# Kernel tuning notes

Measured on AMD Instinct MI355X. Metric: run time of the kernel, lower is better.

## Reference

```python
import jax, jax.numpy as jnp
import numpy as np

B, C, H, W = 4, 256, 56, 56
N = H * W  # 3136 tokens


def setup_inputs() -> dict:
    key = jax.random.key(0)
    ks = jax.random.split(key, 12)
    f = lambda k, s: jax.random.normal(k, s, dtype=jnp.float32)
    return {
        "feat0": f(ks[0], (B, 1, C, H, W)),
        "feat1": f(ks[1], (B, 1, C, H, W)),
        "feat2": f(ks[2], (B, 1, C, H, W)),
        "feat3": f(ks[3], (B, 1, C, H, W)),
        "hist0": jax.random.uniform(ks[4], (B, N), dtype=jnp.float32),
        "hist1": jax.random.uniform(ks[5], (B, N), dtype=jnp.float32),
        "hist2": jax.random.uniform(ks[6], (B, N), dtype=jnp.float32),
        "mask": f(ks[7], (N, N)),
        "Wv": f(ks[8], (C, C)) * 0.02,   # v_linear weight (torch layout [out,in])
        "bv": jnp.zeros((C,), jnp.float32),
        "Wl": f(ks[9], (C, 2 * C)) * 0.02,  # low_channel weight
        "bl": jnp.zeros((C,), jnp.float32),
    }


def _tokens(x5d):
    # [b,1,c,h,w] -> [b, n, c]
    b = x5d.shape[0]
    return x5d.reshape(b, C, N).transpose(0, 2, 1)


def _to5d(tok):
    # [b,n,c] -> [b,1,c,h,w]
    b = tok.shape[0]
    return tok.transpose(0, 2, 1).reshape(b, 1, C, H, W)


def reference(feat0, feat1, feat2, feat3, hist0, hist1, hist2, mask, Wv, bv, Wl, bl):
    scale = 1.0 / jnp.sqrt(jnp.float32(C))

    def stage(q_tok, feat5d):
        f = _tokens(feat5d)                                   # [b,n,c]
        corr = jnp.einsum('bnc,bmc->bnm', q_tok, f) * scale   # [b,n,n]
        p = jax.nn.softmax(corr + mask[None], axis=-1)        # masked softmax
        v = f @ Wv.T + bv                                     # v_linear
        motion = jnp.einsum('bnm,bmc->bnc', p, v)             # attention
        refined = motion + f                                  # residual
        out = jnp.concatenate([refined, f], axis=-1) @ Wl.T + bl  # low_channel
        return refined, out

    # histograms (hist0..hist2) are consumed by the original module but its
    # histogram_mask is dead code; they do not affect the math.
    q = _tokens(feat0)
    refined, out1 = stage(q, feat1)
    refined, out2 = stage(refined, feat2)
    refined, out3 = stage(refined, feat3)

    return jnp.concatenate(
        [feat0, _to5d(out1), _to5d(out2), _to5d(out3)], axis=1
    )  # [b, 4, c, h, w]
```

## Files before the change

kernel.cpp:

```cpp
#include <hip/hip_runtime.h>
#include <hip/hip_bf16.h>

#define B_   4
#define C_   256
#define N_   3136
#define QT_  196
#define NKV_ 98
#define CH_  5

typedef __attribute__((ext_vector_type(8)))  short bf16x8;
typedef __attribute__((ext_vector_type(4)))  float f32x4;
typedef __attribute__((ext_vector_type(16))) float f32x16;

#define LOG2E  1.4426950408889634f
#define SCALE2 (LOG2E / 16.0f)
#define FMAX_  20.0f

__device__ __forceinline__ unsigned short bfbits(float f) {
  __hip_bfloat16 h = __float2bfloat16(f);
  return *(unsigned short*)&h;
}
__device__ __forceinline__ unsigned cvtpk(float lo, float hi) {
  unsigned r;
  asm("v_cvt_pk_bf16_f32 %0, %1, %2" : "=v"(r) : "v"(lo), "v"(hi));
  return r;
}

__device__ __forceinline__ void gld16(const void* g, void* l) {
  __builtin_amdgcn_global_load_lds(
      (const __attribute__((address_space(1))) unsigned int*)g,
      (__attribute__((address_space(3))) unsigned int*)l, 16, 0, 0);
}

__device__ __forceinline__ int vperm(int n) {
  int k = n & 31;
  return (n & ~31) | (k & 16) | (((k >> 2) & 1) << 3) | (k & 3) | (((k >> 3) & 1) << 2);
}

__global__ __launch_bounds__(256) void transpose4_kernel(
    const float* __restrict__ f0, const float* __restrict__ f1,
    const float* __restrict__ f2, const float* __restrict__ f3,
    __hip_bfloat16* __restrict__ d0, __hip_bfloat16* __restrict__ d1,
    __hip_bfloat16* __restrict__ d2, __hip_bfloat16* __restrict__ d3,
    float* __restrict__ out) {
  __shared__ float tile[32][33];
  const int z  = blockIdx.z;
  const int fi = z >> 2;
  const int b  = z & 3;
  const float* src = (fi == 0) ? f0 : (fi == 1) ? f1 : (fi == 2) ? f2 : f3;
  __hip_bfloat16* dst = (fi == 0) ? d0 : (fi == 1) ? d1 : (fi == 2) ? d2 : d3;
  const int n0 = blockIdx.x * 32;
  const int c0 = blockIdx.y * 32;
  const int tx = threadIdx.x & 31;
  const int ty = threadIdx.x >> 5;
  const float* s = src + (size_t)b * C_ * N_;
  float* ob = out + (size_t)b * 4 * C_ * N_;
#pragma unroll
  for (int i = 0; i < 4; ++i) {
    int c = c0 + ty + i * 8;
    float v = s[(size_t)c * N_ + n0 + tx];
    tile[ty + i * 8][tx] = v;
    if (fi == 0) ob[(size_t)c * N_ + n0 + tx] = v;
  }
  __syncthreads();
  __hip_bfloat16* d = dst + (size_t)b * N_ * C_;
#pragma unroll
  for (int i = 0; i < 4; ++i) {
    int n = n0 + ty + i * 8;
    d[(size_t)n * C_ + c0 + tx] = __float2bfloat16(tile[tx][ty + i * 8]);
  }
}

__global__ __launch_bounds__(256) void cvt_all_kernel(
    const float* __restrict__ Wv, const float* __restrict__ Wl,
    const float* __restrict__ mask,
    __hip_bfloat16* __restrict__ Wvb, __hip_bfloat16* __restrict__ Wlb,
    __hip_bfloat16* __restrict__ maskb) {
  int i = blockIdx.x * 256 + threadIdx.x;
  if (i < 24576) {
    const float* src; __hip_bfloat16* dst; int off;
    if (i < 8192) { src = Wv; dst = Wvb; off = i; }
    else          { src = Wl; dst = Wlb; off = i - 8192; }
    const float4* s4 = (const float4*)src;
    float4 a = s4[2 * off], b = s4[2 * off + 1];
    union { unsigned short u[8]; bf16x8 v; } p;
    p.u[0]=bfbits(a.x); p.u[1]=bfbits(a.y); p.u[2]=bfbits(a.z); p.u[3]=bfbits(a.w);
    p.u[4]=bfbits(b.x); p.u[5]=bfbits(b.y); p.u[6]=bfbits(b.z); p.u[7]=bfbits(b.w);
    *(bf16x8*)(dst + 8 * off) = p.v;
    return;
  }
  int j = i - 24576;
  if (j >= NKV_ * NKV_ * 32 * 2) return;
  const int hi  = j & 1;
  const int cl  = (j >> 1) & 31;
  const int rem = j >> 6;
  const int kt  = rem % NKV_;
  const int qu  = rem / NKV_;
  const int q   = qu * 32 + cl;
  const float* s = mask + (size_t)q * N_ + kt * 32 + 4 * hi;
  float4 a0 = *(const float4*)(s);
  float4 a1 = *(const float4*)(s + 8);
  float4 a2 = *(const float4*)(s + 16);
  float4 a3 = *(const float4*)(s + 24);
  union { unsigned short u[16]; bf16x8 v[2]; } p;
  p.u[0]=bfbits(a0.x*LOG2E); p.u[1]=bfbits(a0.y*LOG2E); p.u[2]=bfbits(a0.z*LOG2E); p.u[3]=bfbits(a0.w*LOG2E);
  p.u[4]=bfbits(a1.x*LOG2E); p.u[5]=bfbits(a1.y*LOG2E); p.u[6]=bfbits(a1.z*LOG2E); p.u[7]=bfbits(a1.w*LOG2E);
  p.u[8]=bfbits(a2.x*LOG2E); p.u[9]=bfbits(a2.y*LOG2E); p.u[10]=bfbits(a2.z*LOG2E); p.u[11]=bfbits(a2.w*LOG2E);
  p.u[12]=bfbits(a3.x*LOG2E); p.u[13]=bfbits(a3.y*LOG2E); p.u[14]=bfbits(a3.z*LOG2E); p.u[15]=bfbits(a3.w*LOG2E);
  __hip_bfloat16* d = maskb + ((size_t)rem * 32 + cl) * 32 + hi * 16;
  *(bf16x8*)(d)     = p.v[0];
  *(bf16x8*)(d + 8) = p.v[1];
}

__global__ __launch_bounds__(256) void v_linear_kernel(
    const __hip_bfloat16* __restrict__ f1, const __hip_bfloat16* __restrict__ f2,
    const __hip_bfloat16* __restrict__ f3,
    const __hip_bfloat16* __restrict__ Wv, const float* __restrict__ bv,
    __hip_bfloat16* __restrict__ vT0, __hip_bfloat16* __restrict__ vT1,
    __hip_bfloat16* __restrict__ vT2)
{
  const int s    = blockIdx.z;
  const int b    = blockIdx.y;
  const int nblk = blockIdx.x;
  const __hip_bfloat16* fb = (s == 0) ? f1 : (s == 1) ? f2 : f3;
  __hip_bfloat16* vT = (s == 0) ? vT0 : (s == 1) ? vT1 : vT2;
  const int wave = threadIdx.x >> 6;
  const int lane = threadIdx.x & 63;
  const int qt = lane & 15, g = lane >> 4;
  const int n0 = nblk * 64;
  const __hip_bfloat16* fbb = fb + (size_t)b * N_ * C_;
  const int c0 = wave * 64;
  f32x4 acc[4][4];
#pragma unroll
  for (int u = 0; u < 4; ++u)
#pragma unroll
    for (int j = 0; j < 4; ++j) acc[u][j] = (f32x4){0.f, 0.f, 0.f, 0.f};
#pragma unroll
  for (int kk = 0; kk < 8; ++kk) {
    int ko = kk * 32 + g * 8;
    bf16x8 bb[4];
#pragma unroll
    for (int j = 0; j < 4; ++j)
      bb[j] = *(const bf16x8*)(fbb + (size_t)(n0 + j * 16 + qt) * C_ + ko);
#pragma unroll
    for (int u = 0; u < 4; ++u) {
      bf16x8 a = *(const bf16x8*)(Wv + (size_t)(c0 + u * 16 + qt) * C_ + ko);
#pragma unroll
      for (int j = 0; j < 4; ++j)
        acc[u][j] = __builtin_amdgcn_mfma_f32_16x16x32_bf16(a, bb[j], acc[u][j], 0, 0, 0);
    }
  }
  __hip_bfloat16* outp = vT + (size_t)b * C_ * N_;
#pragma unroll
  for (int u = 0; u < 4; ++u)
#pragma unroll
    for (int j = 0; j < 4; ++j)
#pragma unroll
      for (int r = 0; r < 4; ++r) {
        int c = c0 + u * 16 + 4 * g + r;
        int n = vperm(n0 + j * 16 + qt);
        outp[(size_t)c * N_ + n] = __float2bfloat16(acc[u][j][r] + bv[c]);
      }
}

__global__ __launch_bounds__(256, 2) void attn_kernel(
    const __hip_bfloat16* __restrict__ qb,
    const __hip_bfloat16* __restrict__ kb,
    const __hip_bfloat16* __restrict__ vT,
    const __hip_bfloat16* __restrict__ mb,
    unsigned* __restrict__ pOb,
    float* __restrict__ pML)
{
  __shared__ __hip_bfloat16 Kl[2][32 * 256];
  __shared__ __hip_bfloat16 Vl[2][32 * 256];

  const int bid   = blockIdx.x;
  const int grp   = bid % 20;
  const int qblk  = bid / 20;
  const int b     = grp / CH_;
  const int chunk = grp % CH_;
  const int wave  = threadIdx.x >> 6;
  const int lane  = threadIdx.x & 63;
  const int cl = lane & 31, hi = lane >> 5;
  const int qunit = qblk * 4 + wave;
  const bool valid = qunit < 98;
  const int qu = valid ? qunit : 97;
  const int q0row = qu * 32 + cl;
  const int t0 = (chunk * NKV_) / CH_;
  const int t1 = ((chunk + 1) * NKV_) / CH_;
  const int nt = t1 - t0;
  const int tid = threadIdx.x;

  const __hip_bfloat16* qbb = qb + (size_t)b * N_ * C_;
  const char* kbbc = (const char*)(kb + (size_t)b * N_ * C_);
  const char* vbbc = (const char*)(vT + (size_t)b * C_ * N_);
  const char* mbase = (const char*)mb + (size_t)qu * (NKV_ * 2048) + cl * 64 + hi * 32;

  bf16x8 qa[16];
#pragma unroll
  for (int ks = 0; ks < 16; ++ks)
    qa[ks] = *(const bf16x8*)(qbb + (size_t)q0row * C_ + ks * 16 + 8 * hi);

  f32x16 o[8];
#pragma unroll
  for (int ct = 0; ct < 8; ++ct)
#pragma unroll
    for (int r = 0; r < 16; ++r) o[ct][r] = 0.f;
  float lsum = 0.f;

  auto STAGE = [&](int buf, int t) {
    const char* ks0 = kbbc + (size_t)t * 32 * 512;
#pragma unroll
    for (int i = 0; i < 4; ++i) {
      int g2 = tid + i * 256;
      int ks = g2 >> 6, h2 = (g2 >> 5) & 1, key = g2 & 31;
      gld16(ks0 + key * 512 + ks * 32 + h2 * 16, (char*)&Kl[buf][0] + g2 * 16);
    }
    const char* vs0 = vbbc + (size_t)t * 64;
#pragma unroll
    for (int i = 0; i < 4; ++i) {
      int g2 = tid + i * 256;
      int st = g2 >> 9, h2 = (g2 >> 8) & 1, c = g2 & 255;
      gld16(vs0 + (size_t)c * (N_ * 2) + st * 32 + h2 * 16, (char*)&Vl[buf][0] + g2 * 16);
    }
  };

  union { uint4 v[2]; unsigned w[8]; } mm;
  auto MLOAD = [&](int t) {
    mm.v[0] = *(const uint4*)(mbase + (size_t)t * 2048);
    mm.v[1] = *(const uint4*)(mbase + (size_t)t * 2048 + 16);
  };

  STAGE(0, t0);
  MLOAD(t0);

  const int kread = hi * 512 + cl * 16;
  const int vread = hi * 4096 + cl * 16;

  for (int tt = 0; tt < nt; ++tt) {
    const int buf = tt & 1;
    const bool nl = (tt + 1 < nt);
    if (nl) STAGE(buf ^ 1, t0 + tt + 1);
    if (nl) asm volatile("s_waitcnt vmcnt(10)" ::: "memory");
    else    asm volatile("s_waitcnt vmcnt(2)"  ::: "memory");
    __builtin_amdgcn_s_barrier();

    f32x16 s;
#pragma unroll
    for (int r = 0; r < 16; ++r) s[r] = 0.f;
    if (valid) {
      const char* Kb = (const char*)&Kl[buf][0] + kread;
      __builtin_amdgcn_s_setprio(1);
#pragma unroll
      for (int ks = 0; ks < 16; ++ks) {
        bf16x8 kf = *(const bf16x8*)(Kb + ks * 1024);
        s = __builtin_amdgcn_mfma_f32_32x32x16_bf16(kf, qa[ks], s, 0, 0, 0);
      }
      __builtin_amdgcn_s_setprio(0);
    }
    if (nl) asm volatile("s_waitcnt vmcnt(8)" ::: "memory");
    else    asm volatile("s_waitcnt vmcnt(0)" ::: "memory");

    if (valid) {
      float p[16];
#pragma unroll
      for (int j = 0; j < 16; ++j) {
        unsigned wo = mm.w[j >> 1];
        float mf = __uint_as_float((j & 1) ? (wo & 0xffff0000u) : (wo << 16));
        p[j] = exp2f(fmaf(s[j], SCALE2, mf) - FMAX_);
      }
      lsum += ((p[0]+p[1])+(p[2]+p[3])) + ((p[4]+p[5])+(p[6]+p[7]))
            + ((p[8]+p[9])+(p[10]+p[11])) + ((p[12]+p[13])+(p[14]+p[15]));

      union { unsigned u[4]; bf16x8 v8; } A0, A1;
#pragma unroll
      for (int k = 0; k < 4; ++k) A0.u[k] = cvtpk(p[2 * k], p[2 * k + 1]);
#pragma unroll
      for (int k = 0; k < 4; ++k) A1.u[k] = cvtpk(p[8 + 2 * k], p[9 + 2 * k]);

      const char* Vb = (const char*)&Vl[buf][0] + vread;
      __builtin_amdgcn_s_setprio(1);
#pragma unroll
      for (int ct = 0; ct < 8; ++ct) {
        bf16x8 vf0 = *(const bf16x8*)(Vb + ct * 512);
        o[ct] = __builtin_amdgcn_mfma_f32_32x32x16_bf16(A0.v8, vf0, o[ct], 0, 0, 0);
        bf16x8 vf1 = *(const bf16x8*)(Vb + 8192 + ct * 512);
        o[ct] = __builtin_amdgcn_mfma_f32_32x32x16_bf16(A1.v8, vf1, o[ct], 0, 0, 0);
      }
      __builtin_amdgcn_s_setprio(0);
    }
    if (nl) MLOAD(t0 + tt + 1);
    __builtin_amdgcn_s_barrier();
  }

  if (valid) {
    float lt = lsum + __shfl_xor(lsum, 32);
#pragma unroll
    for (int r = 0; r < 16; ++r) {
      int q = (r & 3) + 8 * (r >> 2) + 4 * hi;
      int qt16 = qu * 2 + (q >> 4);
      int row = q & 15;
      size_t ob = ((((size_t)b * QT_ + qt16) * CH_ + chunk) * 2048) + row * 128 + cl;
#pragma unroll
      for (int pp = 0; pp < 4; ++pp)
        pOb[ob + pp * 32] = cvtpk(o[2 * pp][r], o[2 * pp + 1][r]);
    }
    if (lane < 32) {
      int qt16 = qu * 2 + (cl >> 4);
      int row = cl & 15;
      float* pml = pML + (((size_t)b * QT_ + qt16) * CH_ + chunk) * 32;
      pml[row] = FMAX_;
      pml[16 + row] = lt;
    }
  }
}

__global__ __launch_bounds__(256) void combine_kernel(
    const unsigned* __restrict__ pOb, const float* __restrict__ pML,
    const __hip_bfloat16* __restrict__ fb,
    __hip_bfloat16* __restrict__ ref)
{
  __shared__ float sml[CH_ * 32];
  const int b = blockIdx.y;
  const int qtile = blockIdx.x;
  const int tid = threadIdx.x;
  const float* pml = pML + ((size_t)b * QT_ + qtile) * (CH_ * 32);
  if (tid < CH_ * 32) sml[tid] = pml[tid];
  __syncthreads();

  const int w  = tid & 127;
  const int r0 = (tid >> 7) * 8;
  const int ch_lo = 64 * (w >> 5) + (w & 31);
  const int ch_hi = ch_lo + 32;

  float wgt[CH_][8];
#pragma unroll
  for (int r = 0; r < 8; ++r) {
    int row = r0 + r;
    float M = sml[row];
#pragma unroll
    for (int ch = 1; ch < CH_; ++ch) M = fmaxf(M, sml[ch * 32 + row]);
    float L = 0.f;
#pragma unroll
    for (int ch = 0; ch < CH_; ++ch) {
      float wv = exp2f(sml[ch * 32 + row] - M);
      wgt[ch][r] = wv;
      L += wv * sml[ch * 32 + 16 + row];
    }
    float iL = 1.f / L;
#pragma unroll
    for (int ch = 0; ch < CH_; ++ch) wgt[ch][r] *= iL;
  }

  float acc_lo[8], acc_hi[8];
#pragma unroll
  for (int r = 0; r < 8; ++r) { acc_lo[r] = 0.f; acc_hi[r] = 0.f; }
  const unsigned* base = pOb + ((size_t)b * QT_ + qtile) * (CH_ * 2048) + r0 * 128 + w;
#pragma unroll
  for (int ch = 0; ch < CH_; ++ch) {
    const unsigned* p = base + ch * 2048;
#pragma unroll
    for (int r = 0; r < 8; ++r) {
      unsigned u = p[r * 128];
      acc_lo[r] += wgt[ch][r] * __uint_as_float(u << 16);
      acc_hi[r] += wgt[ch][r] * __uint_as_float(u & 0xffff0000u);
    }
  }

  const __hip_bfloat16* f = fb + ((size_t)b * N_ + qtile * 16 + r0) * C_;
  __hip_bfloat16* rf = ref + ((size_t)b * N_ + qtile * 16 + r0) * C_;
#pragma unroll
  for (int r = 0; r < 8; ++r) {
    rf[r * C_ + ch_lo] = __float2bfloat16(acc_lo[r] + __bfloat162float(f[r * C_ + ch_lo]));
    rf[r * C_ + ch_hi] = __float2bfloat16(acc_hi[r] + __bfloat162float(f[r * C_ + ch_hi]));
  }
}

__global__ __launch_bounds__(256) void out_linear_kernel(
    const __hip_bfloat16* __restrict__ refb,
    const __hip_bfloat16* __restrict__ fb,
    const __hip_bfloat16* __restrict__ Wl,
    const float* __restrict__ bl,
    float* __restrict__ out)
{
  const int b    = blockIdx.z;
  const int cblk = blockIdx.y;
  const int nblk = blockIdx.x;
  const int wave = threadIdx.x >> 6;
  const int lane = threadIdx.x & 63;
  const int qt = lane & 15, g = lane >> 4;
  const int c0 = cblk * 64 + wave * 16;
  const int n0 = nblk * 64;
  const __hip_bfloat16* rb  = refb + (size_t)b * N_ * C_;
  const __hip_bfloat16* fbb = fb  + (size_t)b * N_ * C_;
  f32x4 acc[4];
#pragma unroll
  for (int j = 0; j < 4; ++j) acc[j] = (f32x4){0.f, 0.f, 0.f, 0.f};
#pragma unroll
  for (int kk = 0; kk < 8; ++kk) {
    int ko = kk * 32 + g * 8;
    bf16x8 a = *(const bf16x8*)(Wl + (size_t)(c0 + qt) * 512 + ko);
#pragma unroll
    for (int j = 0; j < 4; ++j) {
      bf16x8 bb = *(const bf16x8*)(rb + (size_t)(n0 + j * 16 + qt) * C_ + ko);
      acc[j] = __builtin_amdgcn_mfma_f32_16x16x32_bf16(a, bb, acc[j], 0, 0, 0);
    }
  }
#pragma unroll
  for (int kk = 0; kk < 8; ++kk) {
    int ko = kk * 32 + g * 8;
    bf16x8 a = *(const bf16x8*)(Wl + (size_t)(c0 + qt) * 512 + 256 + ko);
#pragma unroll
    for (int j = 0; j < 4; ++j) {
      bf16x8 bb = *(const bf16x8*)(fbb + (size_t)(n0 + j * 16 + qt) * C_ + ko);
      acc[j] = __builtin_amdgcn_mfma_f32_16x16x32_bf16(a, bb, acc[j], 0, 0, 0);
    }
  }
  float* ob = out + (size_t)b * 4 * C_ * N_;
#pragma unroll
  for (int j = 0; j < 4; ++j)
#pragma unroll
    for (int r = 0; r < 4; ++r) {
      int c = c0 + 4 * g + r;
      int n = n0 + j * 16 + qt;
      ob[(size_t)c * N_ + n] = acc[j][r] + bl[c];
    }
}

extern "C" void kernel_launch(void* const* d_in, const int* in_sizes, int n_in,
                              void* d_out, int out_size, void* d_ws, size_t ws_size,
                              hipStream_t stream) {
  (void)in_sizes; (void)n_in; (void)out_size; (void)ws_size;
  const float* feat0 = (const float*)d_in[0];
  const float* feat1 = (const float*)d_in[1];
  const float* feat2 = (const float*)d_in[2];
  const float* feat3 = (const float*)d_in[3];
  const float* mask  = (const float*)d_in[7];
  const float* Wv    = (const float*)d_in[8];
  const float* bv    = (const float*)d_in[9];
  const float* Wl    = (const float*)d_in[10];
  const float* bl    = (const float*)d_in[11];
  float* out = (float*)d_out;

  const size_t TOKB = (size_t)B_ * N_ * C_ * 2;
  char* w = (char*)d_ws;
  __hip_bfloat16* q0   = (__hip_bfloat16*)(w);
  __hip_bfloat16* f1   = (__hip_bfloat16*)(w + TOKB);
  __hip_bfloat16* f2   = (__hip_bfloat16*)(w + 2 * TOKB);
  __hip_bfloat16* f3   = (__hip_bfloat16*)(w + 3 * TOKB);
  __hip_bfloat16* vT0  = (__hip_bfloat16*)(w + 4 * TOKB);
  __hip_bfloat16* vT1  = (__hip_bfloat16*)(w + 5 * TOKB);
  __hip_bfloat16* vT2  = (__hip_bfloat16*)(w + 6 * TOKB);
  char* w2 = w + 7 * TOKB;
  __hip_bfloat16* Wv_bf = (__hip_bfloat16*)(w2);
  __hip_bfloat16* Wl_bf = (__hip_bfloat16*)(w2 + 131072);
  __hip_bfloat16* maskb = (__hip_bfloat16*)(w2 + 393216);
  unsigned* pOb         = (unsigned*)(w2 + 393216 + 19668992);
  float* pML            = (float*)(w2 + 393216 + 19668992 + (size_t)B_ * QT_ * CH_ * 4096 * 2);

  dim3 tb(256);
  transpose4_kernel<<<dim3(98, 8, 16), tb, 0, stream>>>(feat0, feat1, feat2, feat3,
                                                        q0, f1, f2, f3, out);
  cvt_all_kernel<<<dim3((24576 + NKV_ * NKV_ * 64 + 255) / 256), tb, 0, stream>>>(
      Wv, Wl, mask, Wv_bf, Wl_bf, maskb);
  v_linear_kernel<<<dim3(49, 4, 3), tb, 0, stream>>>(f1, f2, f3, Wv_bf, bv,
                                                     vT0, vT1, vT2);

  const __hip_bfloat16* fs[3] = {f1, f2, f3};
  const __hip_bfloat16* vTs[3] = {vT0, vT1, vT2};
  __hip_bfloat16* refs[3] = {vT0, vT1, vT0};
  const __hip_bfloat16* q = q0;
  for (int s = 0; s < 3; ++s) {
    attn_kernel<<<dim3(500), tb, 0, stream>>>(q, fs[s], vTs[s], maskb, pOb, pML);
    combine_kernel<<<dim3(196, 4), tb, 0, stream>>>(pOb, pML, fs[s], refs[s]);
    out_linear_kernel<<<dim3(49, 4, 4), tb, 0, stream>>>(refs[s], fs[s], Wl_bf, bl,
                                                         out + (size_t)(s + 1) * C_ * N_);
    q = refs[s];
  }
}
```

Before: 379.1 us.

## Template KV split count, single-buffer V tile, and retile out-linear kernel

The attention kernel is templated on the number of KV chunks and uses 8 splits when the workspace is large enough, falling back to 5. This launches more blocks for better CU fill, at the cost of more partial results for the combine step to merge. The V tile drops from double to single buffering and is now loaded at the start of each iteration, with an extra barrier before P·V. This cuts LDS use but exposes V load latency behind the QK and softmax work. The out-linear kernel is retiled to 32 tokens by 128 channels per block, with both input halves merged into one K loop, changing its grid and reuse pattern.

```diff
diff --git a/kernel.cpp b/kernel.cpp
--- a/kernel.cpp
+++ b/kernel.cpp
@@ -6,7 +6,6 @@
 #define N_   3136
 #define QT_  196
 #define NKV_ 98
-#define CH_  5
 
 typedef __attribute__((ext_vector_type(8)))  short bf16x8;
 typedef __attribute__((ext_vector_type(4)))  float f32x4;
@@ -163,6 +162,7 @@
       }
 }
 
+template<int CH>
 __global__ __launch_bounds__(256, 2) void attn_kernel(
     const __hip_bfloat16* __restrict__ qb,
     const __hip_bfloat16* __restrict__ kb,
@@ -172,13 +172,13 @@
     float* __restrict__ pML)
 {
   __shared__ __hip_bfloat16 Kl[2][32 * 256];
-  __shared__ __hip_bfloat16 Vl[2][32 * 256];
+  __shared__ __hip_bfloat16 Vl[32 * 256];
 
   const int bid   = blockIdx.x;
-  const int grp   = bid % 20;
-  const int qblk  = bid / 20;
-  const int b     = grp / CH_;
-  const int chunk = grp % CH_;
+  const int grp   = bid % (4 * CH);
+  const int qblk  = bid / (4 * CH);
+  const int b     = grp / CH;
+  const int chunk = grp % CH;
   const int wave  = threadIdx.x >> 6;
   const int lane  = threadIdx.x & 63;
   const int cl = lane & 31, hi = lane >> 5;
@@ -186,8 +186,8 @@
   const bool valid = qunit < 98;
   const int qu = valid ? qunit : 97;
   const int q0row = qu * 32 + cl;
-  const int t0 = (chunk * NKV_) / CH_;
-  const int t1 = ((chunk + 1) * NKV_) / CH_;
+  const int t0 = (chunk * NKV_) / CH;
+  const int t1 = ((chunk + 1) * NKV_) / CH;
   const int nt = t1 - t0;
   const int tid = threadIdx.x;
 
@@ -208,7 +208,7 @@
     for (int r = 0; r < 16; ++r) o[ct][r] = 0.f;
   float lsum = 0.f;
 
-  auto STAGE = [&](int buf, int t) {
+  auto STAGE_K = [&](int buf, int t) {
     const char* ks0 = kbbc + (size_t)t * 32 * 512;
 #pragma unroll
     for (int i = 0; i < 4; ++i) {
@@ -216,12 +216,14 @@
       int ks = g2 >> 6, h2 = (g2 >> 5) & 1, key = g2 & 31;
       gld16(ks0 + key * 512 + ks * 32 + h2 * 16, (char*)&Kl[buf][0] + g2 * 16);
     }
+  };
+  auto STAGE_V = [&](int t) {
     const char* vs0 = vbbc + (size_t)t * 64;
 #pragma unroll
     for (int i = 0; i < 4; ++i) {
       int g2 = tid + i * 256;
       int st = g2 >> 9, h2 = (g2 >> 8) & 1, c = g2 & 255;
-      gld16(vs0 + (size_t)c * (N_ * 2) + st * 32 + h2 * 16, (char*)&Vl[buf][0] + g2 * 16);
+      gld16(vs0 + (size_t)c * (N_ * 2) + st * 32 + h2 * 16, (char*)&Vl[0] + g2 * 16);
     }
   };
 
@@ -231,25 +233,26 @@
     mm.v[1] = *(const uint4*)(mbase + (size_t)t * 2048 + 16);
   };
 
-  STAGE(0, t0);
+  STAGE_K(0, t0);
   MLOAD(t0);
 
   const int kread = hi * 512 + cl * 16;
   const int vread = hi * 4096 + cl * 16;
 
   for (int tt = 0; tt < nt; ++tt) {
-    const int buf = tt & 1;
     const bool nl = (tt + 1 < nt);
-    if (nl) STAGE(buf ^ 1, t0 + tt + 1);
-    if (nl) asm volatile("s_waitcnt vmcnt(10)" ::: "memory");
-    else    asm volatile("s_waitcnt vmcnt(2)"  ::: "memory");
+    STAGE_V(t0 + tt);
+    if (nl) STAGE_K((tt + 1) & 1, t0 + tt + 1);
+    if (nl) asm volatile("s_waitcnt vmcnt(8)" ::: "memory");
+    else    asm volatile("s_waitcnt vmcnt(4)" ::: "memory");
     __builtin_amdgcn_s_barrier();
 
     f32x16 s;
 #pragma unroll
     for (int r = 0; r < 16; ++r) s[r] = 0.f;
+    union { unsigned u[4]; bf16x8 v8; } A0, A1;
     if (valid) {
-      const char* Kb = (const char*)&Kl[buf][0] + kread;
+      const char* Kb = (const char*)&Kl[tt & 1][0] + kread;
       __builtin_amdgcn_s_setprio(1);
 #pragma unroll
       for (int ks = 0; ks < 16; ++ks) {
@@ -257,11 +260,6 @@
         s = __builtin_amdgcn_mfma_f32_32x32x16_bf16(kf, qa[ks], s, 0, 0, 0);
       }
       __builtin_amdgcn_s_setprio(0);
-    }
-    if (nl) asm volatile("s_waitcnt vmcnt(8)" ::: "memory");
-    else    asm volatile("s_waitcnt vmcnt(0)" ::: "memory");
-
-    if (valid) {
       float p[16];
 #pragma unroll
       for (int j = 0; j < 16; ++j) {
@@ -271,14 +269,17 @@
       }
       lsum += ((p[0]+p[1])+(p[2]+p[3])) + ((p[4]+p[5])+(p[6]+p[7]))
             + ((p[8]+p[9])+(p[10]+p[11])) + ((p[12]+p[13])+(p[14]+p[15]));
-
-      union { unsigned u[4]; bf16x8 v8; } A0, A1;
 #pragma unroll
       for (int k = 0; k < 4; ++k) A0.u[k] = cvtpk(p[2 * k], p[2 * k + 1]);
 #pragma unroll
       for (int k = 0; k < 4; ++k) A1.u[k] = cvtpk(p[8 + 2 * k], p[9 + 2 * k]);
-
-      const char* Vb = (const char*)&Vl[buf][0] + vread;
+    }
+    if (nl) asm volatile("s_waitcnt vmcnt(4)" ::: "memory");
+    else    asm volatile("s_waitcnt vmcnt(0)" ::: "memory");
+    __builtin_amdgcn_s_barrier();
+
+    if (valid) {
+      const char* Vb = (const char*)&Vl[0] + vread;
       __builtin_amdgcn_s_setprio(1);
 #pragma unroll
       for (int ct = 0; ct < 8; ++ct) {
@@ -300,7 +301,7 @@
       int q = (r & 3) + 8 * (r >> 2) + 4 * hi;
       int qt16 = qu * 2 + (q >> 4);
       int row = q & 15;
-      size_t ob = ((((size_t)b * QT_ + qt16) * CH_ + chunk) * 2048) + row * 128 + cl;
+      size_t ob = ((((size_t)b * QT_ + qt16) * CH + chunk) * 2048) + row * 128 + cl;
 #pragma unroll
       for (int pp = 0; pp < 4; ++pp)
         pOb[ob + pp * 32] = cvtpk(o[2 * pp][r], o[2 * pp + 1][r]);
@@ -308,24 +309,25 @@
     if (lane < 32) {
       int qt16 = qu * 2 + (cl >> 4);
       int row = cl & 15;
-      float* pml = pML + (((size_t)b * QT_ + qt16) * CH_ + chunk) * 32;
+      float* pml = pML + (((size_t)b * QT_ + qt16) * CH + chunk) * 32;
       pml[row] = FMAX_;
       pml[16 + row] = lt;
     }
   }
 }
 
+template<int CH>
 __global__ __launch_bounds__(256) void combine_kernel(
     const unsigned* __restrict__ pOb, const float* __restrict__ pML,
     const __hip_bfloat16* __restrict__ fb,
     __hip_bfloat16* __restrict__ ref)
 {
-  __shared__ float sml[CH_ * 32];
+  __shared__ float sml[CH * 32];
   const int b = blockIdx.y;
   const int qtile = blockIdx.x;
   const int tid = threadIdx.x;
-  const float* pml = pML + ((size_t)b * QT_ + qtile) * (CH_ * 32);
-  if (tid < CH_ * 32) sml[tid] = pml[tid];
+  const float* pml = pML + ((size_t)b * QT_ + qtile) * (CH * 32);
+  if (tid < CH * 32) sml[tid] = pml[tid];
   __syncthreads();
 
   const int w  = tid & 127;
@@ -333,31 +335,31 @@
   const int ch_lo = 64 * (w >> 5) + (w & 31);
   const int ch_hi = ch_lo + 32;
 
-  float wgt[CH_][8];
+  float wgt[CH][8];
 #pragma unroll
   for (int r = 0; r < 8; ++r) {
     int row = r0 + r;
     float M = sml[row];
 #pragma unroll
-    for (int ch = 1; ch < CH_; ++ch) M = fmaxf(M, sml[ch * 32 + row]);
+    for (int ch = 1; ch < CH; ++ch) M = fmaxf(M, sml[ch * 32 + row]);
     float L = 0.f;
 #pragma unroll
-    for (int ch = 0; ch < CH_; ++ch) {
+    for (int ch = 0; ch < CH; ++ch) {
       float wv = exp2f(sml[ch * 32 + row] - M);
       wgt[ch][r] = wv;
       L += wv * sml[ch * 32 + 16 + row];
     }
     float iL = 1.f / L;
 #pragma unroll
-    for (int ch = 0; ch < CH_; ++ch) wgt[ch][r] *= iL;
+    for (int ch = 0; ch < CH; ++ch) wgt[ch][r] *= iL;
   }
 
   float acc_lo[8], acc_hi[8];
 #pragma unroll
   for (int r = 0; r < 8; ++r) { acc_lo[r] = 0.f; acc_hi[r] = 0.f; }
-  const unsigned* base = pOb + ((size_t)b * QT_ + qtile) * (CH_ * 2048) + r0 * 128 + w;
-#pragma unroll
-  for (int ch = 0; ch < CH_; ++ch) {
+  const unsigned* base = pOb + ((size_t)b * QT_ + qtile) * (CH * 2048) + r0 * 128 + w;
+#pragma unroll
+  for (int ch = 0; ch < CH; ++ch) {
     const unsigned* p = base + ch * 2048;
 #pragma unroll
     for (int r = 0; r < 8; ++r) {
@@ -389,48 +391,46 @@
   const int wave = threadIdx.x >> 6;
   const int lane = threadIdx.x & 63;
   const int qt = lane & 15, g = lane >> 4;
-  const int c0 = cblk * 64 + wave * 16;
-  const int n0 = nblk * 64;
+  const int c0 = cblk * 128 + wave * 32;
+  const int n0 = nblk * 32;
   const __hip_bfloat16* rb  = refb + (size_t)b * N_ * C_;
   const __hip_bfloat16* fbb = fb  + (size_t)b * N_ * C_;
-  f32x4 acc[4];
-#pragma unroll
-  for (int j = 0; j < 4; ++j) acc[j] = (f32x4){0.f, 0.f, 0.f, 0.f};
-#pragma unroll
-  for (int kk = 0; kk < 8; ++kk) {
+  f32x4 acc[2][2];
+#pragma unroll
+  for (int u = 0; u < 2; ++u)
+#pragma unroll
+    for (int j = 0; j < 2; ++j) acc[u][j] = (f32x4){0.f, 0.f, 0.f, 0.f};
+#pragma unroll
+  for (int kk = 0; kk < 16; ++kk) {
     int ko = kk * 32 + g * 8;
-    bf16x8 a = *(const bf16x8*)(Wl + (size_t)(c0 + qt) * 512 + ko);
-#pragma unroll
-    for (int j = 0; j < 4; ++j) {
-      bf16x8 bb = *(const bf16x8*)(rb + (size_t)(n0 + j * 16 + qt) * C_ + ko);
-      acc[j] = __builtin_amdgcn_mfma_f32_16x16x32_bf16(a, bb, acc[j], 0, 0, 0);
-    }
-  }
-#pragma unroll
-  for (int kk = 0; kk < 8; ++kk) {
-    int ko = kk * 32 + g * 8;
-    bf16x8 a = *(const bf16x8*)(Wl + (size_t)(c0 + qt) * 512 + 256 + ko);
-#pragma unroll
-    for (int j = 0; j < 4; ++j) {
-      bf16x8 bb = *(const bf16x8*)(fbb + (size_t)(n0 + j * 16 + qt) * C_ + ko);
-      acc[j] = __builtin_amdgcn_mfma_f32_16x16x32_bf16(a, bb, acc[j], 0, 0, 0);
+    const __hip_bfloat16* src = (kk < 8) ? rb : fbb;
+    int ko2 = ko & 255;
+    bf16x8 bb0 = *(const bf16x8*)(src + (size_t)(n0 + qt) * C_ + ko2);
+    bf16x8 bb1 = *(const bf16x8*)(src + (size_t)(n0 + 16 + qt) * C_ + ko2);
+#pragma unroll
+    for (int u = 0; u < 2; ++u) {
+      bf16x8 a = *(const bf16x8*)(Wl + (size_t)(c0 + u * 16 + qt) * 512 + ko);
+      acc[u][0] = __builtin_amdgcn_mfma_f32_16x16x32_bf16(a, bb0, acc[u][0], 0, 0, 0);
+      acc[u][1] = __builtin_amdgcn_mfma_f32_16x16x32_bf16(a, bb1, acc[u][1], 0, 0, 0);
     }
   }
   float* ob = out + (size_t)b * 4 * C_ * N_;
 #pragma unroll
-  for (int j = 0; j < 4; ++j)
-#pragma unroll
-    for (int r = 0; r < 4; ++r) {
-      int c = c0 + 4 * g + r;
-      int n = n0 + j * 16 + qt;
-      ob[(size_t)c * N_ + n] = acc[j][r] + bl[c];
-    }
+  for (int u = 0; u < 2; ++u)
+#pragma unroll
+    for (int j = 0; j < 2; ++j)
+#pragma unroll
+      for (int r = 0; r < 4; ++r) {
+        int c = c0 + u * 16 + 4 * g + r;
+        int n = n0 + j * 16 + qt;
+        ob[(size_t)c * N_ + n] = acc[u][j][r] + bl[c];
+      }
 }
 
 extern "C" void kernel_launch(void* const* d_in, const int* in_sizes, int n_in,
                               void* d_out, int out_size, void* d_ws, size_t ws_size,
                               hipStream_t stream) {
-  (void)in_sizes; (void)n_in; (void)out_size; (void)ws_size;
+  (void)in_sizes; (void)n_in; (void)out_size;
   const float* feat0 = (const float*)d_in[0];
   const float* feat1 = (const float*)d_in[1];
   const float* feat2 = (const float*)d_in[2];
@@ -455,8 +455,14 @@
   __hip_bfloat16* Wv_bf = (__hip_bfloat16*)(w2);
   __hip_bfloat16* Wl_bf = (__hip_bfloat16*)(w2 + 131072);
   __hip_bfloat16* maskb = (__hip_bfloat16*)(w2 + 393216);
-  unsigned* pOb         = (unsigned*)(w2 + 393216 + 19668992);
-  float* pML            = (float*)(w2 + 393216 + 19668992 + (size_t)B_ * QT_ * CH_ * 4096 * 2);
+  char* wp = w2 + 393216 + 19668992;
+  unsigned* pOb = (unsigned*)wp;
+
+  const size_t baseNeed = 7 * TOKB + 393216 + 19668992;
+  const size_t need8 = baseNeed + (size_t)B_ * QT_ * 8 * 8192 + (size_t)B_ * QT_ * 8 * 128;
+  const bool big = ws_size >= need8;
+  const int CH = big ? 8 : 5;
+  float* pML = (float*)(wp + (size_t)B_ * QT_ * CH * 8192);
 
   dim3 tb(256);
   transpose4_kernel<<<dim3(98, 8, 16), tb, 0, stream>>>(feat0, feat1, feat2, feat3,
@@ -471,9 +477,14 @@
   __hip_bfloat16* refs[3] = {vT0, vT1, vT0};
   const __hip_bfloat16* q = q0;
   for (int s = 0; s < 3; ++s) {
-    attn_kernel<<<dim3(500), tb, 0, stream>>>(q, fs[s], vTs[s], maskb, pOb, pML);
-    combine_kernel<<<dim3(196, 4), tb, 0, stream>>>(pOb, pML, fs[s], refs[s]);
-    out_linear_kernel<<<dim3(49, 4, 4), tb, 0, stream>>>(refs[s], fs[s], Wl_bf, bl,
+    if (big) {
+      attn_kernel<8><<<dim3(25 * 4 * 8), tb, 0, stream>>>(q, fs[s], vTs[s], maskb, pOb, pML);
+      combine_kernel<8><<<dim3(196, 4), tb, 0, stream>>>(pOb, pML, fs[s], refs[s]);
+    } else {
+      attn_kernel<5><<<dim3(25 * 4 * 5), tb, 0, stream>>>(q, fs[s], vTs[s], maskb, pOb, pML);
+      combine_kernel<5><<<dim3(196, 4), tb, 0, stream>>>(pOb, pML, fs[s], refs[s]);
+    }
+    out_linear_kernel<<<dim3(98, 2, 4), tb, 0, stream>>>(refs[s], fs[s], Wl_bf, bl,
                                                          out + (size_t)(s + 1) * C_ * N_);
     q = refs[s];
   }
```

Result: slower. 482.4 us (+27.3%).
